# Optimization experiments

Hardware: AMD Instinct MI355X
Metric: run time of the kernel (lower is better)

## Reference

```python
import jax, jax.numpy as jnp
import numpy as np

B, N, K = 8, 512, 16            # batches, proposals per batch, knn neighbors
C_POOL = 256                    # pooled feature dim (hardcoded 256 in source)
G_MLP = [128, 128]              # GLOBAL_INFORMATION.MLP_LAYERS
IN_DIM = C_POOL + G_MLP[-1]     # gnn_input_dim = 384
LAYERS = [512, 512, 512]


def _xavier(key, shape):
    fan_out, fan_in = shape
    lim = np.sqrt(6.0 / (fan_in + fan_out))
    return jax.random.uniform(key, shape, jnp.float32, -lim, lim)


def setup_inputs() -> dict:
    key = jax.random.key(0)
    ks = jax.random.split(key, 12)
    rois = jax.random.normal(ks[0], (B, N, 7), jnp.float32)
    rois = rois.at[:, :, :3].multiply(20.0)  # spread box centers spatially
    pooled_features = jax.random.normal(ks[1], (B, N, C_POOL), jnp.float32)

    # knn_graph per batch (loop=False): edges (neighbor j -> center i)
    coords = rois[:, :, :3]
    d2 = jnp.sum((coords[:, :, None, :] - coords[:, None, :, :]) ** 2, -1)  # [B,N,N]
    d2 = d2 + jnp.eye(N, dtype=jnp.float32) * 1e9                           # no self loops
    _, nbr = jax.lax.top_k(-d2, K)                                          # [B,N,K]
    offs = (jnp.arange(B) * N)[:, None, None]
    src = (nbr + offs).reshape(-1)
    dst = (jnp.broadcast_to(jnp.arange(N)[None, :, None], (B, N, K)) + offs).reshape(-1)
    edge_index = jnp.stack([src, dst]).astype(jnp.int32)                    # [2, B*N*K]

    # global-information MLP params: Linear(7,128), Linear(128,128)
    gW1 = _xavier(ks[2], (G_MLP[0], 7)); gb1 = jnp.zeros((G_MLP[0],), jnp.float32)
    gW2 = _xavier(ks[3], (G_MLP[1], G_MLP[0])); gb2 = jnp.zeros((G_MLP[1],), jnp.float32)

    # EdgeConv fc params: in = 2*in_dim of layer
    fcW1 = _xavier(ks[4], (LAYERS[0], 2 * IN_DIM)); fcb1 = jnp.zeros((LAYERS[0],), jnp.float32)
    fcW2 = _xavier(ks[5], (LAYERS[1], 2 * LAYERS[0])); fcb2 = jnp.zeros((LAYERS[1],), jnp.float32)
    fcW3 = _xavier(ks[6], (LAYERS[2], 2 * LAYERS[1])); fcb3 = jnp.zeros((LAYERS[2],), jnp.float32)

    return dict(rois=rois, pooled_features=pooled_features, edge_index=edge_index,
                gW1=gW1, gb1=gb1, gW2=gW2, gb2=gb2,
                fcW1=fcW1, fcb1=fcb1, fcW2=fcW2, fcb2=fcb2, fcW3=fcW3, fcb3=fcb3)


def reference(rois, pooled_features, edge_index,
              gW1, gb1, gW2, gb2,
              fcW1, fcb1, fcW2, fcb2, fcW3, fcb3):
    # global information MLP on proposal boxes
    g = jax.nn.relu(rois @ gW1.T + gb1)
    g = jax.nn.relu(g @ gW2.T + gb2)                      # [B,N,128]
    x = jnp.concatenate([pooled_features, g], -1).reshape(-1, IN_DIM)  # [B*N, 384]

    src, dst = edge_index[0], edge_index[1]
    n_nodes = B * N
    feats = [x]
    for W, b in ((fcW1, fcb1), (fcW2, fcb2), (fcW3, fcb3)):
        x_i = x[dst]                                      # target features [E,d]
        x_j = x[src]                                      # source features [E,d]
        msg = jax.nn.relu(jnp.concatenate([x_j - x_i, x_i], -1) @ W.T + b)  # [E,out]
        x = jax.ops.segment_max(msg, dst, num_segments=n_nodes)  # scatter-max aggr
        feats.append(x)
    return jnp.concatenate(feats, -1)                     # [B*N, 384+512*3]
```

## Files before the change

### kernel.cpp

```cpp
#include <hip/hip_runtime.h>
#include <hip/hip_bf16.h>

#define BN_NODES 4096
#define KNN 16
#define C_POOL 256
#define G_DIM 128
#define IN_DIM 384
#define L_DIM 512
#define OUT_STRIDE 1920

#define X0_OFF 0
#define X1_OFF 384
#define X2_OFF 896
#define X3_OFF 1408

typedef __attribute__((ext_vector_type(8))) __bf16 bf16x8;
typedef __attribute__((ext_vector_type(4))) float floatx4;

static __device__ __forceinline__ ushort f2bf(float v) {
  return __builtin_bit_cast(ushort, __float2bfloat16(v));
}
static __device__ __forceinline__ float bf2f(ushort u) {
  return __builtin_bit_cast(float, ((unsigned)u) << 16);
}

__global__ __launch_bounds__(256) void node_feat_kernel(
    const float* __restrict__ rois, const float* __restrict__ pooled,
    const float* __restrict__ gW1, const float* __restrict__ gb1,
    const float* __restrict__ gW2, const float* __restrict__ gb2,
    float* __restrict__ out, ushort* __restrict__ Xb) {
  const int nb = blockIdx.x * 8;
  const int t = threadIdx.x;
  const int c = t & 127;
  const int nh = t >> 7;
  __shared__ float rs[8 * 7];
  __shared__ __align__(16) float h1[8][G_DIM];
  if (t < 56) rs[t] = rois[(size_t)nb * 7 + t];
  __syncthreads();
  {
    float w1[7];
#pragma unroll
    for (int i = 0; i < 7; i++) w1[i] = gW1[c * 7 + i];
    float b1 = gb1[c];
#pragma unroll
    for (int n = nh * 4; n < nh * 4 + 4; n++) {
      float a = b1;
#pragma unroll
      for (int i = 0; i < 7; i++) a += rs[n * 7 + i] * w1[i];
      h1[n][c] = fmaxf(a, 0.f);
    }
  }
  __syncthreads();
  float acc[4];
  {
    float b2 = gb2[c];
#pragma unroll
    for (int n = 0; n < 4; n++) acc[n] = b2;
    const float4* w4 = (const float4*)(gW2 + (size_t)c * G_DIM);
#pragma unroll 4
    for (int kc = 0; kc < G_DIM / 4; kc++) {
      float4 wv = w4[kc];
#pragma unroll
      for (int n = 0; n < 4; n++) {
        float4 hv = ((const float4*)h1[nh * 4 + n])[kc];
        acc[n] += wv.x * hv.x + wv.y * hv.y + wv.z * hv.z + wv.w * hv.w;
      }
    }
  }
#pragma unroll
  for (int n = 0; n < 4; n++) {
    int node = nb + nh * 4 + n;
    float g = fmaxf(acc[n], 0.f);
    const float* prow = pooled + (size_t)node * C_POOL;
    float p0 = prow[c], p1 = prow[G_DIM + c];
    float* orow = out + (size_t)node * OUT_STRIDE;
    orow[c] = p0;
    orow[G_DIM + c] = p1;
    orow[C_POOL + c] = g;
    ushort* xrow = Xb + (size_t)node * IN_DIM;
    xrow[c] = f2bf(p0);
    xrow[G_DIM + c] = f2bf(p1);
    xrow[C_POOL + c] = f2bf(g);
  }
}

__global__ __launch_bounds__(128) void wconv_all_kernel(
    const float* __restrict__ W0, const float* __restrict__ W1,
    const float* __restrict__ W2, ushort* __restrict__ Wb0,
    ushort* __restrict__ Wb1, ushort* __restrict__ Wb2) {
  int l = blockIdx.z;
  int j = blockIdx.y;
  int k = blockIdx.x * 128 + threadIdx.x;
  int K = (l == 0) ? IN_DIM : L_DIM;
  if (k >= K) return;
  const float* W = (l == 0) ? W0 : (l == 1) ? W1 : W2;
  ushort* Wb = (l == 0) ? Wb0 : (l == 1) ? Wb1 : Wb2;
  float v = (j < 512) ? W[(size_t)j * (2 * K) + k]
                      : W[(size_t)(j - 512) * (2 * K) + K + k];
  Wb[(size_t)j * K + k] = f2bf(v);
}

__global__ __launch_bounds__(256) void mfma_gemm_kernel(
    const ushort* __restrict__ Xb, const ushort* __restrict__ Wb, int K,
    ushort* __restrict__ PQb) {
  __shared__ ushort sA[128 * 64];
  __shared__ ushort sB[64 * 64];
  const int tid = threadIdx.x;
  const int lane = tid & 63;
  const int w = tid >> 6;
  const int wm = w >> 1, wn = w & 1;
  const int fr = lane & 15;
  const int kc = lane >> 4;
  const int bm = blockIdx.x, bn = blockIdx.y;

  floatx4 acc[4][2];
#pragma unroll
  for (int i = 0; i < 4; i++)
#pragma unroll
    for (int j = 0; j < 2; j++) acc[i][j] = (floatx4){0.f, 0.f, 0.f, 0.f};

  for (int k0 = 0; k0 < K; k0 += 64) {
#pragma unroll
    for (int r = 0; r < 4; r++) {
      int t = w + r * 4;
      int rt = t & 7, ks = t >> 3;
      const ushort* ga =
          Xb + (size_t)(bm * 128 + rt * 16 + fr) * K + k0 + ks * 32 + kc * 8;
      __builtin_amdgcn_global_load_lds(
          (const __attribute__((address_space(1))) void*)ga,
          (__attribute__((address_space(3))) void*)&sA[t * 512 + lane * 8], 16,
          0, 0);
    }
#pragma unroll
    for (int r = 0; r < 2; r++) {
      int t = w + r * 4;
      int ct = t & 3, ks = t >> 2;
      const ushort* gb =
          Wb + (size_t)(bn * 64 + ct * 16 + fr) * K + k0 + ks * 32 + kc * 8;
      __builtin_amdgcn_global_load_lds(
          (const __attribute__((address_space(1))) void*)gb,
          (__attribute__((address_space(3))) void*)&sB[t * 512 + lane * 8], 16,
          0, 0);
    }
    __syncthreads();
#pragma unroll
    for (int ks = 0; ks < 2; ks++) {
      bf16x8 af[4], bf[2];
#pragma unroll
      for (int i = 0; i < 4; i++)
        af[i] = *(const bf16x8*)&sA[(ks * 8 + wm * 4 + i) * 512 + lane * 8];
#pragma unroll
      for (int j = 0; j < 2; j++)
        bf[j] = *(const bf16x8*)&sB[(ks * 4 + wn * 2 + j) * 512 + lane * 8];
#pragma unroll
      for (int i = 0; i < 4; i++)
#pragma unroll
        for (int j = 0; j < 2; j++)
          acc[i][j] = __builtin_amdgcn_mfma_f32_16x16x32_bf16(af[i], bf[j],
                                                              acc[i][j], 0, 0,
                                                              0);
    }
    __syncthreads();
  }

  const int rowB = bm * 128 + wm * 64 + kc * 4;
  const int colB = bn * 64 + wn * 32 + fr;
#pragma unroll
  for (int i = 0; i < 4; i++)
#pragma unroll
    for (int j = 0; j < 2; j++)
#pragma unroll
      for (int r = 0; r < 4; r++)
        PQb[(size_t)(rowB + i * 16 + r) * 1024 + colB + j * 16] =
            f2bf(acc[i][j][r]);
}

__global__ __launch_bounds__(128) void edge_kernel(
    const ushort* __restrict__ PQb, const int* __restrict__ src,
    const float* __restrict__ bias, float* __restrict__ out, int out_off,
    ushort* __restrict__ Xb) {
  int n = blockIdx.x;
  int t = threadIdx.x;
  __shared__ int s[KNN];
  if (t < KNN) s[t] = src[n * KNN + t];
  __syncthreads();
  const ushort* row = PQb + (size_t)n * 1024;
  ushort4 pu = *(const ushort4*)(row + t * 4);
  ushort4 qu = *(const ushort4*)(row + 512 + t * 4);
  float4 bb = ((const float4*)bias)[t];
  float bx = bf2f(qu.x) - bf2f(pu.x) + bb.x;
  float by = bf2f(qu.y) - bf2f(pu.y) + bb.y;
  float bz = bf2f(qu.z) - bf2f(pu.z) + bb.z;
  float bw = bf2f(qu.w) - bf2f(pu.w) + bb.w;
  float mx = -1e30f, my = -1e30f, mz = -1e30f, mw = -1e30f;
#pragma unroll
  for (int k = 0; k < KNN; k++) {
    ushort4 u = *(const ushort4*)(PQb + (size_t)s[k] * 1024 + t * 4);
    mx = fmaxf(mx, bf2f(u.x));
    my = fmaxf(my, bf2f(u.y));
    mz = fmaxf(mz, bf2f(u.z));
    mw = fmaxf(mw, bf2f(u.w));
  }
  float4 res;
  res.x = fmaxf(mx + bx, 0.f);
  res.y = fmaxf(my + by, 0.f);
  res.z = fmaxf(mz + bz, 0.f);
  res.w = fmaxf(mw + bw, 0.f);
  float* orow = out + (size_t)n * OUT_STRIDE + out_off;
  ((float4*)orow)[t] = res;
  ushort4 pk;
  pk.x = f2bf(res.x);
  pk.y = f2bf(res.y);
  pk.z = f2bf(res.z);
  pk.w = f2bf(res.w);
  ((ushort4*)(Xb + (size_t)n * L_DIM))[t] = pk;
}

extern "C" void kernel_launch(void* const* d_in, const int* in_sizes, int n_in,
                              void* d_out, int out_size, void* d_ws,
                              size_t ws_size, hipStream_t stream) {
  const float* rois = (const float*)d_in[0];
  const float* pooled = (const float*)d_in[1];
  const int* edge_index = (const int*)d_in[2];
  const float* gW1 = (const float*)d_in[3];
  const float* gb1 = (const float*)d_in[4];
  const float* gW2 = (const float*)d_in[5];
  const float* gb2 = (const float*)d_in[6];
  const float* fcW[3] = {(const float*)d_in[7], (const float*)d_in[9],
                         (const float*)d_in[11]};
  const float* fcb[3] = {(const float*)d_in[8], (const float*)d_in[10],
                         (const float*)d_in[12]};
  float* out = (float*)d_out;
  const int* src = edge_index;

  char* ws = (char*)d_ws;
  ushort* PQb = (ushort*)ws;
  ushort* Xb = (ushort*)(ws + (size_t)8 * 1024 * 1024);
  ushort* Wb[3] = {(ushort*)(ws + (size_t)12 * 1024 * 1024),
                   (ushort*)(ws + (size_t)13 * 1024 * 1024),
                   (ushort*)(ws + (size_t)14 * 1024 * 1024)};

  wconv_all_kernel<<<dim3(4, 1024, 3), 128, 0, stream>>>(
      fcW[0], fcW[1], fcW[2], Wb[0], Wb[1], Wb[2]);
  node_feat_kernel<<<BN_NODES / 8, 256, 0, stream>>>(rois, pooled, gW1, gb1,
                                                     gW2, gb2, out, Xb);

  const int out_off[3] = {X1_OFF, X2_OFF, X3_OFF};
  const int Kdim[3] = {IN_DIM, L_DIM, L_DIM};

  for (int l = 0; l < 3; l++) {
    mfma_gemm_kernel<<<dim3(32, 16), 256, 0, stream>>>(Xb, Wb[l], Kdim[l],
                                                       PQb);
    edge_kernel<<<BN_NODES, 128, 0, stream>>>(PQb, src, fcb[l], out,
                                              out_off[l], Xb);
  }
}
```

Before: 177.6 us.

## Fuse per-layer GEMM with neighbor max-aggregation in LDS, merge prep kernels

Each EdgeConv layer becomes one kernel. A block takes one batch (512 nodes) and a 16-column output stripe: it computes both the P and Q halves for all 512 nodes with MFMA, stores them in LDS, and runs the 16-neighbor max from LDS, so the PQ round trip through global memory and the separate edge launch go away. The weight bf16 conversion and node-feature kernels are merged into a single prep launch with vectorized conversion, and X buffers are double-buffered across layers. The risks are that the grid shrinks to 256 blocks with large LDS use, which limits occupancy, and that every block reloads the whole batch's activations.

```diff
diff --git a/kernel.cpp b/kernel.cpp
--- a/kernel.cpp
+++ b/kernel.cpp
@@ -23,14 +23,47 @@
 static __device__ __forceinline__ float bf2f(ushort u) {
   return __builtin_bit_cast(float, ((unsigned)u) << 16);
 }
-
-__global__ __launch_bounds__(256) void node_feat_kernel(
+static __device__ __forceinline__ void gld_lds(const ushort* g, ushort* l) {
+  __builtin_amdgcn_global_load_lds(
+      (const __attribute__((address_space(1))) void*)g,
+      (__attribute__((address_space(3))) void*)l, 16, 0, 0);
+}
+
+__global__ __launch_bounds__(256) void prep_kernel(
     const float* __restrict__ rois, const float* __restrict__ pooled,
     const float* __restrict__ gW1, const float* __restrict__ gb1,
     const float* __restrict__ gW2, const float* __restrict__ gb2,
-    float* __restrict__ out, ushort* __restrict__ Xb) {
+    const float* __restrict__ W0, const float* __restrict__ W1,
+    const float* __restrict__ W2, float* __restrict__ out,
+    ushort* __restrict__ Xb0, ushort* __restrict__ Wb0,
+    ushort* __restrict__ Wb1, ushort* __restrict__ Wb2) {
+  const int t = threadIdx.x;
+  if (blockIdx.x >= 512) {
+    int wi = blockIdx.x - 512;
+    const float* W;
+    ushort* Wb;
+    int K, base;
+    if (wi < 384) {
+      W = W0; Wb = Wb0; K = IN_DIM; base = wi;
+    } else if (wi < 896) {
+      W = W1; Wb = Wb1; K = L_DIM; base = wi - 384;
+    } else {
+      W = W2; Wb = Wb2; K = L_DIM; base = wi - 896;
+    }
+    int elem = base * 1024 + t * 4;
+    int j = elem / K;
+    int k = elem - j * K;
+    const float* srcp = (j < 512) ? W + (size_t)j * (2 * K) + k
+                                  : W + (size_t)(j - 512) * (2 * K) + K + k;
+    ushort4 pk;
+    pk.x = f2bf(srcp[0]);
+    pk.y = f2bf(srcp[1]);
+    pk.z = f2bf(srcp[2]);
+    pk.w = f2bf(srcp[3]);
+    *(ushort4*)(Wb + (size_t)j * K + k) = pk;
+    return;
+  }
   const int nb = blockIdx.x * 8;
-  const int t = threadIdx.x;
   const int c = t & 127;
   const int nh = t >> 7;
   __shared__ float rs[8 * 7];
@@ -77,143 +110,122 @@
     orow[c] = p0;
     orow[G_DIM + c] = p1;
     orow[C_POOL + c] = g;
-    ushort* xrow = Xb + (size_t)node * IN_DIM;
+    ushort* xrow = Xb0 + (size_t)node * IN_DIM;
     xrow[c] = f2bf(p0);
     xrow[G_DIM + c] = f2bf(p1);
     xrow[C_POOL + c] = f2bf(g);
   }
 }
 
-__global__ __launch_bounds__(128) void wconv_all_kernel(
-    const float* __restrict__ W0, const float* __restrict__ W1,
-    const float* __restrict__ W2, ushort* __restrict__ Wb0,
-    ushort* __restrict__ Wb1, ushort* __restrict__ Wb2) {
-  int l = blockIdx.z;
-  int j = blockIdx.y;
-  int k = blockIdx.x * 128 + threadIdx.x;
-  int K = (l == 0) ? IN_DIM : L_DIM;
-  if (k >= K) return;
-  const float* W = (l == 0) ? W0 : (l == 1) ? W1 : W2;
-  ushort* Wb = (l == 0) ? Wb0 : (l == 1) ? Wb1 : Wb2;
-  float v = (j < 512) ? W[(size_t)j * (2 * K) + k]
-                      : W[(size_t)(j - 512) * (2 * K) + K + k];
-  Wb[(size_t)j * K + k] = f2bf(v);
-}
-
-__global__ __launch_bounds__(256) void mfma_gemm_kernel(
-    const ushort* __restrict__ Xb, const ushort* __restrict__ Wb, int K,
-    ushort* __restrict__ PQb) {
-  __shared__ ushort sA[128 * 64];
-  __shared__ ushort sB[64 * 64];
+__global__ __launch_bounds__(256) void layer_kernel(
+    const ushort* __restrict__ Xin, int ldx, int K,
+    const ushort* __restrict__ Wb, const int* __restrict__ src,
+    const float* __restrict__ bias, float* __restrict__ out, int out_off,
+    ushort* __restrict__ Xout, int write_x) {
+  __shared__ ushort sA[512 * 64];
+  __shared__ ushort sB[32 * 512];
+  __shared__ ushort sPQ[512 * 32];
+  const int stripe = blockIdx.x;
+  const int b = blockIdx.y;
   const int tid = threadIdx.x;
   const int lane = tid & 63;
   const int w = tid >> 6;
-  const int wm = w >> 1, wn = w & 1;
   const int fr = lane & 15;
   const int kc = lane >> 4;
-  const int bm = blockIdx.x, bn = blockIdx.y;
-
-  floatx4 acc[4][2];
-#pragma unroll
-  for (int i = 0; i < 4; i++)
+
+  const ushort* Ab = Xin + (size_t)(b * 512) * ldx;
+
+  const int nbt = (K >> 5) * 2;
+  for (int r = 0; r < nbt / 4; r++) {
+    int tb = w + 4 * r;
+    int kt = tb >> 1, ct = tb & 1;
+    const ushort* g =
+        Wb + (size_t)(ct * 512 + stripe * 16 + fr) * K + kt * 32 + kc * 8;
+    gld_lds(g, &sB[tb * 512 + lane * 8]);
+  }
+
+  floatx4 acc[8][2];
+#pragma unroll
+  for (int i = 0; i < 8; i++)
 #pragma unroll
     for (int j = 0; j < 2; j++) acc[i][j] = (floatx4){0.f, 0.f, 0.f, 0.f};
 
   for (int k0 = 0; k0 < K; k0 += 64) {
 #pragma unroll
-    for (int r = 0; r < 4; r++) {
-      int t = w + r * 4;
-      int rt = t & 7, ks = t >> 3;
-      const ushort* ga =
-          Xb + (size_t)(bm * 128 + rt * 16 + fr) * K + k0 + ks * 32 + kc * 8;
-      __builtin_amdgcn_global_load_lds(
-          (const __attribute__((address_space(1))) void*)ga,
-          (__attribute__((address_space(3))) void*)&sA[t * 512 + lane * 8], 16,
-          0, 0);
-    }
-#pragma unroll
-    for (int r = 0; r < 2; r++) {
-      int t = w + r * 4;
-      int ct = t & 3, ks = t >> 2;
-      const ushort* gb =
-          Wb + (size_t)(bn * 64 + ct * 16 + fr) * K + k0 + ks * 32 + kc * 8;
-      __builtin_amdgcn_global_load_lds(
-          (const __attribute__((address_space(1))) void*)gb,
-          (__attribute__((address_space(3))) void*)&sB[t * 512 + lane * 8], 16,
-          0, 0);
+    for (int r = 0; r < 16; r++) {
+      int ta = w + 4 * r;
+      int rt = ta >> 1, ks = ta & 1;
+      const ushort* g =
+          Ab + (size_t)(rt * 16 + fr) * ldx + k0 + ks * 32 + kc * 8;
+      gld_lds(g, &sA[ta * 512 + lane * 8]);
     }
     __syncthreads();
 #pragma unroll
     for (int ks = 0; ks < 2; ks++) {
-      bf16x8 af[4], bf[2];
-#pragma unroll
-      for (int i = 0; i < 4; i++)
-        af[i] = *(const bf16x8*)&sA[(ks * 8 + wm * 4 + i) * 512 + lane * 8];
-#pragma unroll
-      for (int j = 0; j < 2; j++)
-        bf[j] = *(const bf16x8*)&sB[(ks * 4 + wn * 2 + j) * 512 + lane * 8];
-#pragma unroll
-      for (int i = 0; i < 4; i++)
-#pragma unroll
-        for (int j = 0; j < 2; j++)
-          acc[i][j] = __builtin_amdgcn_mfma_f32_16x16x32_bf16(af[i], bf[j],
-                                                              acc[i][j], 0, 0,
-                                                              0);
+      int ktg = (k0 >> 5) + ks;
+      bf16x8 bfv[2];
+#pragma unroll
+      for (int ct = 0; ct < 2; ct++)
+        bfv[ct] = *(const bf16x8*)&sB[(ktg * 2 + ct) * 512 + lane * 8];
+#pragma unroll
+      for (int rl = 0; rl < 8; rl++) {
+        bf16x8 av = *(const bf16x8*)&sA[((w * 8 + rl) * 2 + ks) * 512 + lane * 8];
+#pragma unroll
+        for (int ct = 0; ct < 2; ct++)
+          acc[rl][ct] = __builtin_amdgcn_mfma_f32_16x16x32_bf16(av, bfv[ct],
+                                                                acc[rl][ct], 0,
+                                                                0, 0);
+      }
     }
     __syncthreads();
   }
 
-  const int rowB = bm * 128 + wm * 64 + kc * 4;
-  const int colB = bn * 64 + wn * 32 + fr;
-#pragma unroll
-  for (int i = 0; i < 4; i++)
-#pragma unroll
-    for (int j = 0; j < 2; j++)
+#pragma unroll
+  for (int rl = 0; rl < 8; rl++)
+#pragma unroll
+    for (int ct = 0; ct < 2; ct++)
 #pragma unroll
       for (int r = 0; r < 4; r++)
-        PQb[(size_t)(rowB + i * 16 + r) * 1024 + colB + j * 16] =
-            f2bf(acc[i][j][r]);
-}
-
-__global__ __launch_bounds__(128) void edge_kernel(
-    const ushort* __restrict__ PQb, const int* __restrict__ src,
-    const float* __restrict__ bias, float* __restrict__ out, int out_off,
-    ushort* __restrict__ Xb) {
-  int n = blockIdx.x;
-  int t = threadIdx.x;
-  __shared__ int s[KNN];
-  if (t < KNN) s[t] = src[n * KNN + t];
+        sPQ[((w * 8 + rl) * 16 + kc * 4 + r) * 32 + ct * 16 + fr] =
+            f2bf(acc[rl][ct][r]);
   __syncthreads();
-  const ushort* row = PQb + (size_t)n * 1024;
-  ushort4 pu = *(const ushort4*)(row + t * 4);
-  ushort4 qu = *(const ushort4*)(row + 512 + t * 4);
-  float4 bb = ((const float4*)bias)[t];
-  float bx = bf2f(qu.x) - bf2f(pu.x) + bb.x;
-  float by = bf2f(qu.y) - bf2f(pu.y) + bb.y;
-  float bz = bf2f(qu.z) - bf2f(pu.z) + bb.z;
-  float bw = bf2f(qu.w) - bf2f(pu.w) + bb.w;
-  float mx = -1e30f, my = -1e30f, mz = -1e30f, mw = -1e30f;
-#pragma unroll
-  for (int k = 0; k < KNN; k++) {
-    ushort4 u = *(const ushort4*)(PQb + (size_t)s[k] * 1024 + t * 4);
-    mx = fmaxf(mx, bf2f(u.x));
-    my = fmaxf(my, bf2f(u.y));
-    mz = fmaxf(mz, bf2f(u.z));
-    mw = fmaxf(mw, bf2f(u.w));
-  }
-  float4 res;
-  res.x = fmaxf(mx + bx, 0.f);
-  res.y = fmaxf(my + by, 0.f);
-  res.z = fmaxf(mz + bz, 0.f);
-  res.w = fmaxf(mw + bw, 0.f);
-  float* orow = out + (size_t)n * OUT_STRIDE + out_off;
-  ((float4*)orow)[t] = res;
-  ushort4 pk;
-  pk.x = f2bf(res.x);
-  pk.y = f2bf(res.y);
-  pk.z = f2bf(res.z);
-  pk.w = f2bf(res.w);
-  ((ushort4*)(Xb + (size_t)n * L_DIM))[t] = pk;
+
+  const int cq = tid & 3;
+  const int slice = tid >> 2;
+  const int c0 = stripe * 16;
+  const float4 bb = *(const float4*)&bias[c0 + cq * 4];
+#pragma unroll
+  for (int i = 0; i < 8; i++) {
+    int n = slice * 8 + i;
+    const int* sp = src + (size_t)(b * 512 + n) * KNN;
+    float mx = -1e30f, my = -1e30f, mz = -1e30f, mw = -1e30f;
+#pragma unroll
+    for (int k = 0; k < KNN; k++) {
+      int sl = sp[k] - b * 512;
+      ushort4 u = *(const ushort4*)&sPQ[sl * 32 + cq * 4];
+      mx = fmaxf(mx, bf2f(u.x));
+      my = fmaxf(my, bf2f(u.y));
+      mz = fmaxf(mz, bf2f(u.z));
+      mw = fmaxf(mw, bf2f(u.w));
+    }
+    ushort4 pu = *(const ushort4*)&sPQ[n * 32 + cq * 4];
+    ushort4 qu = *(const ushort4*)&sPQ[n * 32 + 16 + cq * 4];
+    float4 res;
+    res.x = fmaxf(mx - bf2f(pu.x) + bf2f(qu.x) + bb.x, 0.f);
+    res.y = fmaxf(my - bf2f(pu.y) + bf2f(qu.y) + bb.y, 0.f);
+    res.z = fmaxf(mz - bf2f(pu.z) + bf2f(qu.z) + bb.z, 0.f);
+    res.w = fmaxf(mw - bf2f(pu.w) + bf2f(qu.w) + bb.w, 0.f);
+    size_t node = (size_t)(b * 512 + n);
+    *(float4*)(out + node * OUT_STRIDE + out_off + c0 + cq * 4) = res;
+    if (write_x) {
+      ushort4 pk;
+      pk.x = f2bf(res.x);
+      pk.y = f2bf(res.y);
+      pk.z = f2bf(res.z);
+      pk.w = f2bf(res.w);
+      *(ushort4*)(Xout + node * L_DIM + c0 + cq * 4) = pk;
+    }
+  }
 }
 
 extern "C" void kernel_launch(void* const* d_in, const int* in_sizes, int n_in,
@@ -234,24 +246,21 @@
   const int* src = edge_index;
 
   char* ws = (char*)d_ws;
-  ushort* PQb = (ushort*)ws;
-  ushort* Xb = (ushort*)(ws + (size_t)8 * 1024 * 1024);
-  ushort* Wb[3] = {(ushort*)(ws + (size_t)12 * 1024 * 1024),
-                   (ushort*)(ws + (size_t)13 * 1024 * 1024),
-                   (ushort*)(ws + (size_t)14 * 1024 * 1024)};
-
-  wconv_all_kernel<<<dim3(4, 1024, 3), 128, 0, stream>>>(
-      fcW[0], fcW[1], fcW[2], Wb[0], Wb[1], Wb[2]);
-  node_feat_kernel<<<BN_NODES / 8, 256, 0, stream>>>(rois, pooled, gW1, gb1,
-                                                     gW2, gb2, out, Xb);
-
-  const int out_off[3] = {X1_OFF, X2_OFF, X3_OFF};
-  const int Kdim[3] = {IN_DIM, L_DIM, L_DIM};
-
-  for (int l = 0; l < 3; l++) {
-    mfma_gemm_kernel<<<dim3(32, 16), 256, 0, stream>>>(Xb, Wb[l], Kdim[l],
-                                                       PQb);
-    edge_kernel<<<BN_NODES, 128, 0, stream>>>(PQb, src, fcb[l], out,
-                                              out_off[l], Xb);
-  }
-}
+  ushort* Xb0 = (ushort*)ws;
+  ushort* Xb1 = (ushort*)(ws + (size_t)4 * 1024 * 1024);
+  ushort* Xb2 = (ushort*)(ws + (size_t)8 * 1024 * 1024);
+  ushort* Wb0 = (ushort*)(ws + (size_t)12 * 1024 * 1024);
+  ushort* Wb1 = (ushort*)(ws + (size_t)13 * 1024 * 1024);
+  ushort* Wb2 = (ushort*)(ws + (size_t)14 * 1024 * 1024);
+
+  prep_kernel<<<1920, 256, 0, stream>>>(rois, pooled, gW1, gb1, gW2, gb2,
+                                        fcW[0], fcW[1], fcW[2], out, Xb0, Wb0,
+                                        Wb1, Wb2);
+  layer_kernel<<<dim3(32, 8), 256, 0, stream>>>(Xb0, IN_DIM, IN_DIM, Wb0, src,
+                                                fcb[0], out, X1_OFF, Xb1, 1);
+  layer_kernel<<<dim3(32, 8), 256, 0, stream>>>(Xb1, L_DIM, L_DIM, Wb1, src,
+                                                fcb[1], out, X2_OFF, Xb2, 1);
+  layer_kernel<<<dim3(32, 8), 256, 0, stream>>>(Xb2, L_DIM, L_DIM, Wb2, src,
+                                                fcb[2], out, X3_OFF, nullptr,
+                                                0);
+}
```

Measured after the change: 183.2 us. 1.03x slower.

## Merge weight conversion into node-feature prep kernel and use 8-wave GEMM blocks

Applied to the files above, without the earlier changes.

Folds the weight fp32-to-bf16 conversion kernel into the node-feature kernel as extra blocks, so both run in a single launch, and vectorises the conversion to four elements per thread. Doubles the GEMM block to 512 threads (8 waves), each wave computing a 32x32 subtile instead of 64x32, with an adjusted LDS tile indexing. The intent is to remove one launch and raise per-CU parallelism in the GEMM, at the cost of less register-level reuse per wave.

```diff
diff --git a/kernel.cpp b/kernel.cpp
--- a/kernel.cpp
+++ b/kernel.cpp
@@ -23,14 +23,47 @@
 static __device__ __forceinline__ float bf2f(ushort u) {
   return __builtin_bit_cast(float, ((unsigned)u) << 16);
 }
-
-__global__ __launch_bounds__(256) void node_feat_kernel(
+static __device__ __forceinline__ void gld_lds(const ushort* g, ushort* l) {
+  __builtin_amdgcn_global_load_lds(
+      (const __attribute__((address_space(1))) void*)g,
+      (__attribute__((address_space(3))) void*)l, 16, 0, 0);
+}
+
+__global__ __launch_bounds__(256) void prep_kernel(
     const float* __restrict__ rois, const float* __restrict__ pooled,
     const float* __restrict__ gW1, const float* __restrict__ gb1,
     const float* __restrict__ gW2, const float* __restrict__ gb2,
-    float* __restrict__ out, ushort* __restrict__ Xb) {
+    const float* __restrict__ W0, const float* __restrict__ W1,
+    const float* __restrict__ W2, float* __restrict__ out,
+    ushort* __restrict__ Xb0, ushort* __restrict__ Wb0,
+    ushort* __restrict__ Wb1, ushort* __restrict__ Wb2) {
+  const int t = threadIdx.x;
+  if (blockIdx.x >= 512) {
+    int wi = blockIdx.x - 512;
+    const float* W;
+    ushort* Wb;
+    int K, base;
+    if (wi < 384) {
+      W = W0; Wb = Wb0; K = IN_DIM; base = wi;
+    } else if (wi < 896) {
+      W = W1; Wb = Wb1; K = L_DIM; base = wi - 384;
+    } else {
+      W = W2; Wb = Wb2; K = L_DIM; base = wi - 896;
+    }
+    int elem = base * 1024 + t * 4;
+    int j = elem / K;
+    int k = elem - j * K;
+    const float* srcp = (j < 512) ? W + (size_t)j * (2 * K) + k
+                                  : W + (size_t)(j - 512) * (2 * K) + K + k;
+    ushort4 pk;
+    pk.x = f2bf(srcp[0]);
+    pk.y = f2bf(srcp[1]);
+    pk.z = f2bf(srcp[2]);
+    pk.w = f2bf(srcp[3]);
+    *(ushort4*)(Wb + (size_t)j * K + k) = pk;
+    return;
+  }
   const int nb = blockIdx.x * 8;
-  const int t = threadIdx.x;
   const int c = t & 127;
   const int nh = t >> 7;
   __shared__ float rs[8 * 7];
@@ -77,30 +110,14 @@
     orow[c] = p0;
     orow[G_DIM + c] = p1;
     orow[C_POOL + c] = g;
-    ushort* xrow = Xb + (size_t)node * IN_DIM;
+    ushort* xrow = Xb0 + (size_t)node * IN_DIM;
     xrow[c] = f2bf(p0);
     xrow[G_DIM + c] = f2bf(p1);
     xrow[C_POOL + c] = f2bf(g);
   }
 }
 
-__global__ __launch_bounds__(128) void wconv_all_kernel(
-    const float* __restrict__ W0, const float* __restrict__ W1,
-    const float* __restrict__ W2, ushort* __restrict__ Wb0,
-    ushort* __restrict__ Wb1, ushort* __restrict__ Wb2) {
-  int l = blockIdx.z;
-  int j = blockIdx.y;
-  int k = blockIdx.x * 128 + threadIdx.x;
-  int K = (l == 0) ? IN_DIM : L_DIM;
-  if (k >= K) return;
-  const float* W = (l == 0) ? W0 : (l == 1) ? W1 : W2;
-  ushort* Wb = (l == 0) ? Wb0 : (l == 1) ? Wb1 : Wb2;
-  float v = (j < 512) ? W[(size_t)j * (2 * K) + k]
-                      : W[(size_t)(j - 512) * (2 * K) + K + k];
-  Wb[(size_t)j * K + k] = f2bf(v);
-}
-
-__global__ __launch_bounds__(256) void mfma_gemm_kernel(
+__global__ __launch_bounds__(512) void mfma_gemm_kernel(
     const ushort* __restrict__ Xb, const ushort* __restrict__ Wb, int K,
     ushort* __restrict__ PQb) {
   __shared__ ushort sA[128 * 64];
@@ -108,52 +125,46 @@
   const int tid = threadIdx.x;
   const int lane = tid & 63;
   const int w = tid >> 6;
-  const int wm = w >> 1, wn = w & 1;
+  const int wm = w >> 1;
+  const int wn = w & 1;
   const int fr = lane & 15;
   const int kc = lane >> 4;
   const int bm = blockIdx.x, bn = blockIdx.y;
 
-  floatx4 acc[4][2];
-#pragma unroll
-  for (int i = 0; i < 4; i++)
+  floatx4 acc[2][2];
+#pragma unroll
+  for (int i = 0; i < 2; i++)
 #pragma unroll
     for (int j = 0; j < 2; j++) acc[i][j] = (floatx4){0.f, 0.f, 0.f, 0.f};
 
   for (int k0 = 0; k0 < K; k0 += 64) {
 #pragma unroll
-    for (int r = 0; r < 4; r++) {
-      int t = w + r * 4;
-      int rt = t & 7, ks = t >> 3;
+    for (int r = 0; r < 2; r++) {
+      int ta = w + r * 8;
+      int rt = ta >> 1, ks = ta & 1;
       const ushort* ga =
           Xb + (size_t)(bm * 128 + rt * 16 + fr) * K + k0 + ks * 32 + kc * 8;
-      __builtin_amdgcn_global_load_lds(
-          (const __attribute__((address_space(1))) void*)ga,
-          (__attribute__((address_space(3))) void*)&sA[t * 512 + lane * 8], 16,
-          0, 0);
-    }
-#pragma unroll
-    for (int r = 0; r < 2; r++) {
-      int t = w + r * 4;
-      int ct = t & 3, ks = t >> 2;
+      gld_lds(ga, &sA[ta * 512 + lane * 8]);
+    }
+    {
+      int tb = w;
+      int ct = tb >> 1, ks = tb & 1;
       const ushort* gb =
           Wb + (size_t)(bn * 64 + ct * 16 + fr) * K + k0 + ks * 32 + kc * 8;
-      __builtin_amdgcn_global_load_lds(
-          (const __attribute__((address_space(1))) void*)gb,
-          (__attribute__((address_space(3))) void*)&sB[t * 512 + lane * 8], 16,
-          0, 0);
+      gld_lds(gb, &sB[tb * 512 + lane * 8]);
     }
     __syncthreads();
 #pragma unroll
     for (int ks = 0; ks < 2; ks++) {
-      bf16x8 af[4], bf[2];
-#pragma unroll
-      for (int i = 0; i < 4; i++)
-        af[i] = *(const bf16x8*)&sA[(ks * 8 + wm * 4 + i) * 512 + lane * 8];
+      bf16x8 af[2], bf[2];
+#pragma unroll
+      for (int i = 0; i < 2; i++)
+        af[i] = *(const bf16x8*)&sA[((wm * 2 + i) * 2 + ks) * 512 + lane * 8];
 #pragma unroll
       for (int j = 0; j < 2; j++)
-        bf[j] = *(const bf16x8*)&sB[(ks * 4 + wn * 2 + j) * 512 + lane * 8];
-#pragma unroll
-      for (int i = 0; i < 4; i++)
+        bf[j] = *(const bf16x8*)&sB[((wn * 2 + j) * 2 + ks) * 512 + lane * 8];
+#pragma unroll
+      for (int i = 0; i < 2; i++)
 #pragma unroll
         for (int j = 0; j < 2; j++)
           acc[i][j] = __builtin_amdgcn_mfma_f32_16x16x32_bf16(af[i], bf[j],
@@ -163,10 +174,10 @@
     __syncthreads();
   }
 
-  const int rowB = bm * 128 + wm * 64 + kc * 4;
+  const int rowB = bm * 128 + wm * 32 + kc * 4;
   const int colB = bn * 64 + wn * 32 + fr;
 #pragma unroll
-  for (int i = 0; i < 4; i++)
+  for (int i = 0; i < 2; i++)
 #pragma unroll
     for (int j = 0; j < 2; j++)
 #pragma unroll
@@ -240,16 +251,15 @@
                    (ushort*)(ws + (size_t)13 * 1024 * 1024),
                    (ushort*)(ws + (size_t)14 * 1024 * 1024)};
 
-  wconv_all_kernel<<<dim3(4, 1024, 3), 128, 0, stream>>>(
-      fcW[0], fcW[1], fcW[2], Wb[0], Wb[1], Wb[2]);
-  node_feat_kernel<<<BN_NODES / 8, 256, 0, stream>>>(rois, pooled, gW1, gb1,
-                                                     gW2, gb2, out, Xb);
+  prep_kernel<<<1920, 256, 0, stream>>>(rois, pooled, gW1, gb1, gW2, gb2,
+                                        fcW[0], fcW[1], fcW[2], out, Xb, Wb[0],
+                                        Wb[1], Wb[2]);
 
   const int out_off[3] = {X1_OFF, X2_OFF, X3_OFF};
   const int Kdim[3] = {IN_DIM, L_DIM, L_DIM};
 
   for (int l = 0; l < 3; l++) {
-    mfma_gemm_kernel<<<dim3(32, 16), 256, 0, stream>>>(Xb, Wb[l], Kdim[l],
+    mfma_gemm_kernel<<<dim3(32, 16), 512, 0, stream>>>(Xb, Wb[l], Kdim[l],
                                                        PQb);
     edge_kernel<<<BN_NODES, 128, 0, stream>>>(PQb, src, fcb[l], out,
                                               out_off[l], Xb);
```

New measurement: 170.1 us. 4.2% less time.
